# Kernel tuning notes

Measured on AMD Instinct MI355X. Metric: run time of the kernel, lower is better.

The kernel has to match this reference:

```python
import jax, jax.numpy as jnp
import numpy as np

H = 64  # hidden_size
E = 100  # ebd_size
MAX_LEN = 100


def setup_inputs() -> dict:
    key = jax.random.key(0)
    ks = jax.random.split(key, 7)
    B, L = 4096, 100
    return {
        "x": jax.random.normal(ks[0], (B, L, E), jnp.float32),
        "W_in": jax.random.normal(ks[1], (E, 3 * H), jnp.float32) * 0.1,
        "b_in": jax.random.normal(ks[2], (3 * H,), jnp.float32) * 0.1,
        "W_h": jax.random.normal(ks[3], (H, 3 * H), jnp.float32) * 0.1,
        "b_h": jax.random.normal(ks[4], (3 * H,), jnp.float32) * 0.1,
        "W_fc": jax.random.normal(ks[5], (H, 2), jnp.float32) * 0.1,
        "b_fc": jax.random.normal(ks[6], (2,), jnp.float32) * 0.1,
    }


def _standardize(t):
    # torch: (t - t.mean(1, keepdim)) / t.std(1, keepdim)  (std is unbiased, ddof=1)
    m = jnp.mean(t, axis=1, keepdims=True)
    s = jnp.std(t, axis=1, keepdims=True, ddof=1)
    return (t - m) / s


def _gru_step(h, xt, W_in, b_in, W_h, b_h, norm):
    ti = xt @ W_in + b_in            # [B, 3H]
    th = h @ W_h + b_h               # [B, 3H]
    if norm:
        ti = _standardize(ti)
        th = _standardize(th)
    r_i, z_i, n_i = jnp.split(ti, 3, axis=1)
    r_h, z_h, n_h = jnp.split(th, 3, axis=1)
    r_t = jax.nn.sigmoid(r_i + r_h)
    z_t = jax.nn.sigmoid(z_i + z_h)
    n_t = jnp.tanh(n_i + r_t * n_h)
    return (1.0 - z_t) * n_t + z_t * h


def reference(x, W_in, b_in, W_h, b_h, W_fc, b_fc):
    B, L, _ = x.shape
    L_eff = min(L, MAX_LEN + 1)  # loop breaks when l > max_length
    xs = jnp.transpose(x[:, :L_eff, :], (1, 0, 2))  # [L, B, E]
    h0 = jnp.zeros((B, H), x.dtype)

    # loop 1: no norm
    h1, _ = jax.lax.scan(
        lambda h, xt: (_gru_step(h, xt, W_in, b_in, W_h, b_h, norm=False), None),
        h0, xs)
    # loop 2: vector norm; note original code does NOT reset hid_i
    h2, _ = jax.lax.scan(
        lambda h, xt: (_gru_step(h, xt, W_in, b_in, W_h, b_h, norm=True), None),
        h1, xs)
    return h2 @ W_fc + b_fc
```

## Files before the change

kernel.cpp:

```cpp
#include <hip/hip_runtime.h>

#define L_SEQ 100
#define E_DIM 100
#define G_DIM 192
#define B_TOT 4096

typedef __attribute__((ext_vector_type(8))) short bf16x8;
typedef __attribute__((ext_vector_type(4))) float f32x4;
typedef __attribute__((ext_vector_type(4))) float float4v;
typedef __attribute__((ext_vector_type(4))) unsigned uint4v;
typedef __attribute__((ext_vector_type(2))) unsigned uint2v;

static __device__ __forceinline__ unsigned short f2bf(float f) {
    union { float f; unsigned u; } v; v.f = f;
    unsigned r = v.u + 0x7FFFu + ((v.u >> 16) & 1u);
    return (unsigned short)(r >> 16);
}
static __device__ __forceinline__ unsigned cvtpk(float lo, float hi) {
    unsigned r;
    asm("v_cvt_pk_bf16_f32 %0, %1, %2" : "=v"(r) : "v"(lo), "v"(hi));
    return r;
}
static __device__ __forceinline__ bf16x8 as_bf16x8(uint4v u) {
    union { uint4v u; bf16x8 h; } v; v.u = u; return v.h;
}
static __device__ __forceinline__ float sigmoidf_(float x) { return 1.f / (1.f + __expf(-x)); }
static __device__ __forceinline__ float tanhf_(float x)    { return 1.f - 2.f / (__expf(2.f * x) + 1.f); }

#define BAR() do { \
    asm volatile("s_waitcnt lgkmcnt(0)" ::: "memory"); \
    __builtin_amdgcn_s_barrier(); \
    asm volatile("" ::: "memory"); \
} while (0)

struct XBuf { f32x4 v[6]; f32x4 tail; };

static __device__ __forceinline__ void x_pf(
    XBuf& b, const float* __restrict__ xlane, const float* __restrict__ xrow, int s2, bool g0)
{
    int t = (s2 < L_SEQ) ? s2 : (s2 - L_SEQ);
    if (t > L_SEQ - 1) t = L_SEQ - 1;
    const float* p = xlane + t * E_DIM;
    b.v[0] = *(const f32x4*)(p);
    b.v[1] = *(const f32x4*)(p + 4);
    b.v[2] = *(const f32x4*)(p + 32);
    b.v[3] = *(const f32x4*)(p + 36);
    b.v[4] = *(const f32x4*)(p + 64);
    b.v[5] = *(const f32x4*)(p + 68);
    const f32x4 z = {0.f, 0.f, 0.f, 0.f};
    b.tail = g0 ? *(const f32x4*)(xrow + t * E_DIM + 96) : z;
}

template<int PHASE>
static __device__ __forceinline__ void rstep(
    XBuf& xb, const float* __restrict__ xlane, const float* __restrict__ xrow, int s,
    unsigned short (&hs)[2][16][72], float (&sl)[2][16][4][4],
    const bf16x8 (&awin)[3][4], const bf16x8 (&awh)[3][2],
    const float (&binq)[12], const float (&bhq)[12],
    float (&hreg)[4], int w, int g, int c16, bool g0)
{
    bf16x8 bx0 = as_bf16x8((uint4v){cvtpk(xb.v[0][0], xb.v[0][1]), cvtpk(xb.v[0][2], xb.v[0][3]),
                                    cvtpk(xb.v[1][0], xb.v[1][1]), cvtpk(xb.v[1][2], xb.v[1][3])});
    bf16x8 bx1 = as_bf16x8((uint4v){cvtpk(xb.v[2][0], xb.v[2][1]), cvtpk(xb.v[2][2], xb.v[2][3]),
                                    cvtpk(xb.v[3][0], xb.v[3][1]), cvtpk(xb.v[3][2], xb.v[3][3])});
    bf16x8 bx2 = as_bf16x8((uint4v){cvtpk(xb.v[4][0], xb.v[4][1]), cvtpk(xb.v[4][2], xb.v[4][3]),
                                    cvtpk(xb.v[5][0], xb.v[5][1]), cvtpk(xb.v[5][2], xb.v[5][3])});
    bf16x8 bx3 = as_bf16x8((uint4v){cvtpk(xb.tail[0], xb.tail[1]), cvtpk(xb.tail[2], xb.tail[3]),
                                    0u, 0u});
    x_pf(xb, xlane, xrow, s + 2, g0);

    BAR();

    const int p = s & 1;
    bf16x8 h0 = *(const bf16x8*)&hs[p][c16][8 * g];
    bf16x8 h1 = *(const bf16x8*)&hs[p][c16][32 + 8 * g];

    const f32x4 zero = {0.f, 0.f, 0.f, 0.f};
    f32x4 ti0 = __builtin_amdgcn_mfma_f32_16x16x32_bf16(awin[0][0], bx0, zero, 0, 0, 0);
    f32x4 ti1 = __builtin_amdgcn_mfma_f32_16x16x32_bf16(awin[1][0], bx0, zero, 0, 0, 0);
    f32x4 ti2 = __builtin_amdgcn_mfma_f32_16x16x32_bf16(awin[2][0], bx0, zero, 0, 0, 0);
    ti0 = __builtin_amdgcn_mfma_f32_16x16x32_bf16(awin[0][1], bx1, ti0, 0, 0, 0);
    ti1 = __builtin_amdgcn_mfma_f32_16x16x32_bf16(awin[1][1], bx1, ti1, 0, 0, 0);
    ti2 = __builtin_amdgcn_mfma_f32_16x16x32_bf16(awin[2][1], bx1, ti2, 0, 0, 0);
    ti0 = __builtin_amdgcn_mfma_f32_16x16x32_bf16(awin[0][2], bx2, ti0, 0, 0, 0);
    ti1 = __builtin_amdgcn_mfma_f32_16x16x32_bf16(awin[1][2], bx2, ti1, 0, 0, 0);
    ti2 = __builtin_amdgcn_mfma_f32_16x16x32_bf16(awin[2][2], bx2, ti2, 0, 0, 0);
    ti0 = __builtin_amdgcn_mfma_f32_16x16x32_bf16(awin[0][3], bx3, ti0, 0, 0, 0);
    ti1 = __builtin_amdgcn_mfma_f32_16x16x32_bf16(awin[1][3], bx3, ti1, 0, 0, 0);
    ti2 = __builtin_amdgcn_mfma_f32_16x16x32_bf16(awin[2][3], bx3, ti2, 0, 0, 0);
    f32x4 th0 = __builtin_amdgcn_mfma_f32_16x16x32_bf16(awh[0][0], h0, zero, 0, 0, 0);
    f32x4 th1 = __builtin_amdgcn_mfma_f32_16x16x32_bf16(awh[1][0], h0, zero, 0, 0, 0);
    f32x4 th2 = __builtin_amdgcn_mfma_f32_16x16x32_bf16(awh[2][0], h0, zero, 0, 0, 0);
    th0 = __builtin_amdgcn_mfma_f32_16x16x32_bf16(awh[0][1], h1, th0, 0, 0, 0);
    th1 = __builtin_amdgcn_mfma_f32_16x16x32_bf16(awh[1][1], h1, th1, 0, 0, 0);
    th2 = __builtin_amdgcn_mfma_f32_16x16x32_bf16(awh[2][1], h1, th2, 0, 0, 0);

    float a[12], b[12];
    #pragma unroll
    for (int rr = 0; rr < 4; ++rr) {
        a[rr]     = ti0[rr] + binq[rr];
        a[4 + rr] = ti1[rr] + binq[4 + rr];
        a[8 + rr] = ti2[rr] + binq[8 + rr];
        b[rr]     = th0[rr] + bhq[rr];
        b[4 + rr] = th1[rr] + bhq[4 + rr];
        b[8 + rr] = th2[rr] + bhq[8 + rr];
    }

    float mti = 0.f, rti = 1.f, mth = 0.f, rth = 1.f;
    if constexpr (PHASE) {
        float sti = 0.f, ssti = 0.f, sth = 0.f, ssth = 0.f;
        #pragma unroll
        for (int k = 0; k < 12; ++k) {
            sti += a[k]; ssti = fmaf(a[k], a[k], ssti);
            sth += b[k]; ssth = fmaf(b[k], b[k], ssth);
        }
        sti += __shfl_xor(sti, 16); sti += __shfl_xor(sti, 32);
        ssti += __shfl_xor(ssti, 16); ssti += __shfl_xor(ssti, 32);
        sth += __shfl_xor(sth, 16); sth += __shfl_xor(sth, 32);
        ssth += __shfl_xor(ssth, 16); ssth += __shfl_xor(ssth, 32);
        if (g == 0) {
            float4v v = {sti, ssti, sth, ssth};
            *(float4v*)&sl[p][c16][w][0] = v;
        }
        BAR();
        float4v q0 = *(const float4v*)&sl[p][c16][0][0];
        float4v q1 = *(const float4v*)&sl[p][c16][1][0];
        float4v q2 = *(const float4v*)&sl[p][c16][2][0];
        float4v q3 = *(const float4v*)&sl[p][c16][3][0];
        float S_ti  = q0[0] + q1[0] + q2[0] + q3[0];
        float SS_ti = q0[1] + q1[1] + q2[1] + q3[1];
        float S_th  = q0[2] + q1[2] + q2[2] + q3[2];
        float SS_th = q0[3] + q1[3] + q2[3] + q3[3];
        mti = S_ti * (1.f / G_DIM);
        rti = rsqrtf(fmaxf((SS_ti - (float)G_DIM * mti * mti) * (1.f / (G_DIM - 1)), 1e-24f));
        mth = S_th * (1.f / G_DIM);
        rth = rsqrtf(fmaxf((SS_th - (float)G_DIM * mth * mth) * (1.f / (G_DIM - 1)), 1e-24f));
    }

    float hn[4];
    #pragma unroll
    for (int rr = 0; rr < 4; ++rr) {
        float tir, tiz, tin, thr, thz, thn;
        if constexpr (PHASE) {
            tir = (a[rr]     - mti) * rti;
            tiz = (a[4 + rr] - mti) * rti;
            tin = (a[8 + rr] - mti) * rti;
            thr = (b[rr]     - mth) * rth;
            thz = (b[4 + rr] - mth) * rth;
            thn = (b[8 + rr] - mth) * rth;
        } else {
            tir = a[rr]; tiz = a[4 + rr]; tin = a[8 + rr];
            thr = b[rr]; thz = b[4 + rr]; thn = b[8 + rr];
        }
        float rt = sigmoidf_(tir + thr);
        float zt = sigmoidf_(tiz + thz);
        float nv = tanhf_(tin + rt * thn);
        hn[rr] = (1.f - zt) * nv + zt * hreg[rr];
        hreg[rr] = hn[rr];
    }
    uint2v hv = { cvtpk(hn[0], hn[1]), cvtpk(hn[2], hn[3]) };
    *(uint2v*)&hs[p ^ 1][c16][16 * w + 4 * g] = hv;
}

__global__ __launch_bounds__(256, 1) void gru_fused(
    const float* __restrict__ x,
    const float* __restrict__ Win, const float* __restrict__ bin,
    const float* __restrict__ Wh,  const float* __restrict__ bh,
    const float* __restrict__ Wfc, const float* __restrict__ bfc,
    float* __restrict__ out)
{
    __shared__ unsigned short hs[2][16][72];
    __shared__ float sl[2][16][4][4];

    const int tid = threadIdx.x;
    const int w   = tid >> 6, l = tid & 63;
    const int c16 = l & 15,  g = l >> 4;
    const bool g0 = (g == 0);
    const int row0 = blockIdx.x * 16;

    bf16x8 awin[3][4];
    #pragma unroll
    for (int i = 0; i < 3; ++i)
      #pragma unroll
      for (int kt = 0; kt < 4; ++kt)
        #pragma unroll
        for (int j = 0; j < 8; ++j) {
            int k = 32 * kt + 8 * g + j;
            float v = (k < E_DIM) ? Win[k * G_DIM + 16 * (w + 4 * i) + c16] : 0.f;
            awin[i][kt][j] = (short)f2bf(v);
        }
    bf16x8 awh[3][2];
    #pragma unroll
    for (int i = 0; i < 3; ++i)
      #pragma unroll
      for (int kt = 0; kt < 2; ++kt)
        #pragma unroll
        for (int j = 0; j < 8; ++j)
            awh[i][kt][j] = (short)f2bf(Wh[(32 * kt + 8 * g + j) * G_DIM + 16 * (w + 4 * i) + c16]);

    float binq[12], bhq[12];
    #pragma unroll
    for (int i = 0; i < 3; ++i)
      #pragma unroll
      for (int rr = 0; rr < 4; ++rr) {
          binq[4 * i + rr] = bin[16 * (w + 4 * i) + 4 * g + rr];
          bhq[4 * i + rr]  = bh[16 * (w + 4 * i) + 4 * g + rr];
      }

    {
        bf16x8 z = {0, 0, 0, 0, 0, 0, 0, 0};
        *(bf16x8*)&hs[0][c16][8 * g]      = z;
        *(bf16x8*)&hs[0][c16][32 + 8 * g] = z;
    }

    const float* xrow  = x + (size_t)(row0 + c16) * (L_SEQ * E_DIM);
    const float* xlane = xrow + 8 * g;

    float hreg[4] = {0.f, 0.f, 0.f, 0.f};
    XBuf xA, xB;
    x_pf(xA, xlane, xrow, 0, g0);
    x_pf(xB, xlane, xrow, 1, g0);

    #pragma unroll 1
    for (int s = 0; s < L_SEQ; s += 2) {
        rstep<0>(xA, xlane, xrow, s,     hs, sl, awin, awh, binq, bhq, hreg, w, g, c16, g0);
        rstep<0>(xB, xlane, xrow, s + 1, hs, sl, awin, awh, binq, bhq, hreg, w, g, c16, g0);
    }
    #pragma unroll 1
    for (int s = L_SEQ; s < 2 * L_SEQ; s += 2) {
        rstep<1>(xA, xlane, xrow, s,     hs, sl, awin, awh, binq, bhq, hreg, w, g, c16, g0);
        rstep<1>(xB, xlane, xrow, s + 1, hs, sl, awin, awh, binq, bhq, hreg, w, g, c16, g0);
    }

    float p0 = 0.f, p1 = 0.f;
    #pragma unroll
    for (int rr = 0; rr < 4; ++rr) {
        int c = 16 * w + 4 * g + rr;
        p0 = fmaf(hreg[rr], Wfc[2 * c],     p0);
        p1 = fmaf(hreg[rr], Wfc[2 * c + 1], p1);
    }
    p0 += __shfl_xor(p0, 16); p0 += __shfl_xor(p0, 32);
    p1 += __shfl_xor(p1, 16); p1 += __shfl_xor(p1, 32);
    if (g == 0) {
        sl[0][c16][w][0] = p0;
        sl[0][c16][w][1] = p1;
    }
    BAR();
    if (tid < 16) {
        out[(row0 + tid) * 2 + 0] = sl[0][tid][0][0] + sl[0][tid][1][0] + sl[0][tid][2][0] + sl[0][tid][3][0] + bfc[0];
        out[(row0 + tid) * 2 + 1] = sl[0][tid][0][1] + sl[0][tid][1][1] + sl[0][tid][2][1] + sl[0][tid][3][1] + bfc[1];
    }
}

extern "C" void kernel_launch(void* const* d_in, const int* in_sizes, int n_in,
                              void* d_out, int out_size, void* d_ws, size_t ws_size,
                              hipStream_t stream) {
    const float* x   = (const float*)d_in[0];
    const float* Win = (const float*)d_in[1];
    const float* bin = (const float*)d_in[2];
    const float* Wh  = (const float*)d_in[3];
    const float* bh  = (const float*)d_in[4];
    const float* Wfc = (const float*)d_in[5];
    const float* bfc = (const float*)d_in[6];
    float* out = (float*)d_out;
    gru_fused<<<dim3(B_TOT / 16), dim3(256), 0, stream>>>(
        x, Win, bin, Wh, bh, Wfc, bfc, out);
}
```

Baseline: 239.0 us.

## Split GRU into warp-specialized input-projection producer and recurrent consumer waves

Blocks now have 512 threads. Four producer waves compute the input projection x@W_in, including its bias and the sum and sum-of-squares statistics, one step ahead of time and write the results to double-buffered shared memory. Four consumer waves, running at raised priority, do only the h@W_h MFMAs, the normalization and the gate math on the serial recurrence path. The gate math is also rewritten with rcp/rsq intrinsics and fused normalization constants. The aim is to take the x-load and input-GEMM latency off the critical recurrence chain, at the cost of more shared memory, an extra barrier per step and doubled thread count.

Result: faster. 201.0 us (median of 2 runs) (-15.9%).

```diff
diff --git a/kernel.cpp b/kernel.cpp
--- a/kernel.cpp
+++ b/kernel.cpp
@@ -8,8 +8,11 @@
 typedef __attribute__((ext_vector_type(8))) short bf16x8;
 typedef __attribute__((ext_vector_type(4))) float f32x4;
 typedef __attribute__((ext_vector_type(4))) float float4v;
+typedef __attribute__((ext_vector_type(2))) float float2v;
 typedef __attribute__((ext_vector_type(4))) unsigned uint4v;
 typedef __attribute__((ext_vector_type(2))) unsigned uint2v;
+
+#define MFMA16 __builtin_amdgcn_mfma_f32_16x16x32_bf16
 
 static __device__ __forceinline__ unsigned short f2bf(float f) {
     union { float f; unsigned u; } v; v.f = f;
@@ -24,8 +27,7 @@
 static __device__ __forceinline__ bf16x8 as_bf16x8(uint4v u) {
     union { uint4v u; bf16x8 h; } v; v.u = u; return v.h;
 }
-static __device__ __forceinline__ float sigmoidf_(float x) { return 1.f / (1.f + __expf(-x)); }
-static __device__ __forceinline__ float tanhf_(float x)    { return 1.f - 2.f / (__expf(2.f * x) + 1.f); }
+static __device__ __forceinline__ float rcpf_(float x) { return __builtin_amdgcn_rcpf(x); }
 
 #define BAR() do { \
     asm volatile("s_waitcnt lgkmcnt(0)" ::: "memory"); \
@@ -35,11 +37,17 @@
 
 struct XBuf { f32x4 v[6]; f32x4 tail; };
 
+static __device__ __forceinline__ int tmod(int c) {
+    int t = c;
+    if (t >= L_SEQ) t -= L_SEQ;
+    if (t >= L_SEQ) t -= L_SEQ;
+    return t;
+}
+
 static __device__ __forceinline__ void x_pf(
-    XBuf& b, const float* __restrict__ xlane, const float* __restrict__ xrow, int s2, bool g0)
+    XBuf& b, const float* __restrict__ xlane, const float* __restrict__ xrow, int c, bool g0)
 {
-    int t = (s2 < L_SEQ) ? s2 : (s2 - L_SEQ);
-    if (t > L_SEQ - 1) t = L_SEQ - 1;
+    const int t = tmod(c);
     const float* p = xlane + t * E_DIM;
     b.v[0] = *(const f32x4*)(p);
     b.v[1] = *(const f32x4*)(p + 4);
@@ -51,13 +59,10 @@
     b.tail = g0 ? *(const f32x4*)(xrow + t * E_DIM + 96) : z;
 }
 
-template<int PHASE>
-static __device__ __forceinline__ void rstep(
-    XBuf& xb, const float* __restrict__ xlane, const float* __restrict__ xrow, int s,
-    unsigned short (&hs)[2][16][72], float (&sl)[2][16][4][4],
-    const bf16x8 (&awin)[3][4], const bf16x8 (&awh)[3][2],
-    const float (&binq)[12], const float (&bhq)[12],
-    float (&hreg)[4], int w, int g, int c16, bool g0)
+static __device__ __forceinline__ void produce(
+    XBuf& xb, const float* __restrict__ xlane, const float* __restrict__ xrow,
+    int c, bool g0, float* __restrict__ tird, float* __restrict__ sltiw,
+    const bf16x8 (&awin)[3][4], const float (&binq)[12])
 {
     bf16x8 bx0 = as_bf16x8((uint4v){cvtpk(xb.v[0][0], xb.v[0][1]), cvtpk(xb.v[0][2], xb.v[0][3]),
                                     cvtpk(xb.v[1][0], xb.v[1][1]), cvtpk(xb.v[1][2], xb.v[1][3])});
@@ -67,188 +72,253 @@
                                     cvtpk(xb.v[5][0], xb.v[5][1]), cvtpk(xb.v[5][2], xb.v[5][3])});
     bf16x8 bx3 = as_bf16x8((uint4v){cvtpk(xb.tail[0], xb.tail[1]), cvtpk(xb.tail[2], xb.tail[3]),
                                     0u, 0u});
-    x_pf(xb, xlane, xrow, s + 2, g0);
-
-    BAR();
-
-    const int p = s & 1;
-    bf16x8 h0 = *(const bf16x8*)&hs[p][c16][8 * g];
-    bf16x8 h1 = *(const bf16x8*)&hs[p][c16][32 + 8 * g];
+    x_pf(xb, xlane, xrow, c + 2, g0);
 
     const f32x4 zero = {0.f, 0.f, 0.f, 0.f};
-    f32x4 ti0 = __builtin_amdgcn_mfma_f32_16x16x32_bf16(awin[0][0], bx0, zero, 0, 0, 0);
-    f32x4 ti1 = __builtin_amdgcn_mfma_f32_16x16x32_bf16(awin[1][0], bx0, zero, 0, 0, 0);
-    f32x4 ti2 = __builtin_amdgcn_mfma_f32_16x16x32_bf16(awin[2][0], bx0, zero, 0, 0, 0);
-    ti0 = __builtin_amdgcn_mfma_f32_16x16x32_bf16(awin[0][1], bx1, ti0, 0, 0, 0);
-    ti1 = __builtin_amdgcn_mfma_f32_16x16x32_bf16(awin[1][1], bx1, ti1, 0, 0, 0);
-    ti2 = __builtin_amdgcn_mfma_f32_16x16x32_bf16(awin[2][1], bx1, ti2, 0, 0, 0);
-    ti0 = __builtin_amdgcn_mfma_f32_16x16x32_bf16(awin[0][2], bx2, ti0, 0, 0, 0);
-    ti1 = __builtin_amdgcn_mfma_f32_16x16x32_bf16(awin[1][2], bx2, ti1, 0, 0, 0);
-    ti2 = __builtin_amdgcn_mfma_f32_16x16x32_bf16(awin[2][2], bx2, ti2, 0, 0, 0);
-    ti0 = __builtin_amdgcn_mfma_f32_16x16x32_bf16(awin[0][3], bx3, ti0, 0, 0, 0);
-    ti1 = __builtin_amdgcn_mfma_f32_16x16x32_bf16(awin[1][3], bx3, ti1, 0, 0, 0);
-    ti2 = __builtin_amdgcn_mfma_f32_16x16x32_bf16(awin[2][3], bx3, ti2, 0, 0, 0);
-    f32x4 th0 = __builtin_amdgcn_mfma_f32_16x16x32_bf16(awh[0][0], h0, zero, 0, 0, 0);
-    f32x4 th1 = __builtin_amdgcn_mfma_f32_16x16x32_bf16(awh[1][0], h0, zero, 0, 0, 0);
-    f32x4 th2 = __builtin_amdgcn_mfma_f32_16x16x32_bf16(awh[2][0], h0, zero, 0, 0, 0);
-    th0 = __builtin_amdgcn_mfma_f32_16x16x32_bf16(awh[0][1], h1, th0, 0, 0, 0);
-    th1 = __builtin_amdgcn_mfma_f32_16x16x32_bf16(awh[1][1], h1, th1, 0, 0, 0);
-    th2 = __builtin_amdgcn_mfma_f32_16x16x32_bf16(awh[2][1], h1, th2, 0, 0, 0);
-
-    float a[12], b[12];
+    f32x4 t0 = MFMA16(awin[0][0], bx0, zero, 0, 0, 0);
+    f32x4 t1 = MFMA16(awin[1][0], bx0, zero, 0, 0, 0);
+    f32x4 t2 = MFMA16(awin[2][0], bx0, zero, 0, 0, 0);
+    t0 = MFMA16(awin[0][1], bx1, t0, 0, 0, 0);
+    t1 = MFMA16(awin[1][1], bx1, t1, 0, 0, 0);
+    t2 = MFMA16(awin[2][1], bx1, t2, 0, 0, 0);
+    t0 = MFMA16(awin[0][2], bx2, t0, 0, 0, 0);
+    t1 = MFMA16(awin[1][2], bx2, t1, 0, 0, 0);
+    t2 = MFMA16(awin[2][2], bx2, t2, 0, 0, 0);
+    t0 = MFMA16(awin[0][3], bx3, t0, 0, 0, 0);
+    t1 = MFMA16(awin[1][3], bx3, t1, 0, 0, 0);
+    t2 = MFMA16(awin[2][3], bx3, t2, 0, 0, 0);
+
+    const int par = c & 1;
+    float4v A0 = {t0[0] + binq[0], t0[1] + binq[1], t0[2] + binq[2],  t0[3] + binq[3]};
+    float4v A1 = {t1[0] + binq[4], t1[1] + binq[5], t1[2] + binq[6],  t1[3] + binq[7]};
+    float4v A2 = {t2[0] + binq[8], t2[1] + binq[9], t2[2] + binq[10], t2[3] + binq[11]};
+    float* dst = tird + par * 3328;
+    *(float4v*)(dst)     = A0;
+    *(float4v*)(dst + 4) = A1;
+    *(float4v*)(dst + 8) = A2;
+
+    float s = ((A0[0] + A0[1]) + (A0[2] + A0[3])) + ((A1[0] + A1[1]) + (A1[2] + A1[3]))
+            + ((A2[0] + A2[1]) + (A2[2] + A2[3]));
+    float ss = 0.f;
     #pragma unroll
-    for (int rr = 0; rr < 4; ++rr) {
-        a[rr]     = ti0[rr] + binq[rr];
-        a[4 + rr] = ti1[rr] + binq[4 + rr];
-        a[8 + rr] = ti2[rr] + binq[8 + rr];
-        b[rr]     = th0[rr] + bhq[rr];
-        b[4 + rr] = th1[rr] + bhq[4 + rr];
-        b[8 + rr] = th2[rr] + bhq[8 + rr];
-    }
-
-    float mti = 0.f, rti = 1.f, mth = 0.f, rth = 1.f;
-    if constexpr (PHASE) {
-        float sti = 0.f, ssti = 0.f, sth = 0.f, ssth = 0.f;
-        #pragma unroll
-        for (int k = 0; k < 12; ++k) {
-            sti += a[k]; ssti = fmaf(a[k], a[k], ssti);
-            sth += b[k]; ssth = fmaf(b[k], b[k], ssth);
-        }
-        sti += __shfl_xor(sti, 16); sti += __shfl_xor(sti, 32);
-        ssti += __shfl_xor(ssti, 16); ssti += __shfl_xor(ssti, 32);
-        sth += __shfl_xor(sth, 16); sth += __shfl_xor(sth, 32);
-        ssth += __shfl_xor(ssth, 16); ssth += __shfl_xor(ssth, 32);
-        if (g == 0) {
-            float4v v = {sti, ssti, sth, ssth};
-            *(float4v*)&sl[p][c16][w][0] = v;
-        }
-        BAR();
-        float4v q0 = *(const float4v*)&sl[p][c16][0][0];
-        float4v q1 = *(const float4v*)&sl[p][c16][1][0];
-        float4v q2 = *(const float4v*)&sl[p][c16][2][0];
-        float4v q3 = *(const float4v*)&sl[p][c16][3][0];
-        float S_ti  = q0[0] + q1[0] + q2[0] + q3[0];
-        float SS_ti = q0[1] + q1[1] + q2[1] + q3[1];
-        float S_th  = q0[2] + q1[2] + q2[2] + q3[2];
-        float SS_th = q0[3] + q1[3] + q2[3] + q3[3];
-        mti = S_ti * (1.f / G_DIM);
-        rti = rsqrtf(fmaxf((SS_ti - (float)G_DIM * mti * mti) * (1.f / (G_DIM - 1)), 1e-24f));
-        mth = S_th * (1.f / G_DIM);
-        rth = rsqrtf(fmaxf((SS_th - (float)G_DIM * mth * mth) * (1.f / (G_DIM - 1)), 1e-24f));
-    }
-
-    float hn[4];
+    for (int k2 = 0; k2 < 4; ++k2) ss = fmaf(A0[k2], A0[k2], ss);
     #pragma unroll
-    for (int rr = 0; rr < 4; ++rr) {
-        float tir, tiz, tin, thr, thz, thn;
-        if constexpr (PHASE) {
-            tir = (a[rr]     - mti) * rti;
-            tiz = (a[4 + rr] - mti) * rti;
-            tin = (a[8 + rr] - mti) * rti;
-            thr = (b[rr]     - mth) * rth;
-            thz = (b[4 + rr] - mth) * rth;
-            thn = (b[8 + rr] - mth) * rth;
-        } else {
-            tir = a[rr]; tiz = a[4 + rr]; tin = a[8 + rr];
-            thr = b[rr]; thz = b[4 + rr]; thn = b[8 + rr];
-        }
-        float rt = sigmoidf_(tir + thr);
-        float zt = sigmoidf_(tiz + thz);
-        float nv = tanhf_(tin + rt * thn);
-        hn[rr] = (1.f - zt) * nv + zt * hreg[rr];
-        hreg[rr] = hn[rr];
-    }
-    uint2v hv = { cvtpk(hn[0], hn[1]), cvtpk(hn[2], hn[3]) };
-    *(uint2v*)&hs[p ^ 1][c16][16 * w + 4 * g] = hv;
-}
-
-__global__ __launch_bounds__(256, 1) void gru_fused(
+    for (int k2 = 0; k2 < 4; ++k2) ss = fmaf(A1[k2], A1[k2], ss);
+    #pragma unroll
+    for (int k2 = 0; k2 < 4; ++k2) ss = fmaf(A2[k2], A2[k2], ss);
+    s  += __shfl_xor(s, 16);  s  += __shfl_xor(s, 32);
+    ss += __shfl_xor(ss, 16); ss += __shfl_xor(ss, 32);
+    if (g0) *(float2v*)(sltiw + par * 192) = (float2v){s, ss};
+}
+
+__global__ __launch_bounds__(512, 1) void gru_ws(
     const float* __restrict__ x,
     const float* __restrict__ Win, const float* __restrict__ bin,
     const float* __restrict__ Wh,  const float* __restrict__ bh,
     const float* __restrict__ Wfc, const float* __restrict__ bfc,
     float* __restrict__ out)
 {
-    __shared__ unsigned short hs[2][16][72];
-    __shared__ float sl[2][16][4][4];
+    __shared__ __align__(16) unsigned short hs[2][16][72];
+    __shared__ __align__(16) float tir[2][4][16][52];
+    __shared__ __align__(16) float slti[2][16][12];
+    __shared__ __align__(16) float slth[2][16][12];
 
     const int tid = threadIdx.x;
-    const int w   = tid >> 6, l = tid & 63;
-    const int c16 = l & 15,  g = l >> 4;
+    const int wv  = tid >> 6;
+    const int w   = wv & 3;
+    const bool tirole = (wv >= 4);
+    const int l = tid & 63, c16 = l & 15, g = l >> 4;
     const bool g0 = (g == 0);
     const int row0 = blockIdx.x * 16;
 
-    bf16x8 awin[3][4];
-    #pragma unroll
-    for (int i = 0; i < 3; ++i)
-      #pragma unroll
-      for (int kt = 0; kt < 4; ++kt)
-        #pragma unroll
-        for (int j = 0; j < 8; ++j) {
-            int k = 32 * kt + 8 * g + j;
-            float v = (k < E_DIM) ? Win[k * G_DIM + 16 * (w + 4 * i) + c16] : 0.f;
-            awin[i][kt][j] = (short)f2bf(v);
-        }
-    bf16x8 awh[3][2];
-    #pragma unroll
-    for (int i = 0; i < 3; ++i)
-      #pragma unroll
-      for (int kt = 0; kt < 2; ++kt)
-        #pragma unroll
-        for (int j = 0; j < 8; ++j)
-            awh[i][kt][j] = (short)f2bf(Wh[(32 * kt + 8 * g + j) * G_DIM + 16 * (w + 4 * i) + c16]);
-
-    float binq[12], bhq[12];
-    #pragma unroll
-    for (int i = 0; i < 3; ++i)
-      #pragma unroll
-      for (int rr = 0; rr < 4; ++rr) {
-          binq[4 * i + rr] = bin[16 * (w + 4 * i) + 4 * g + rr];
-          bhq[4 * i + rr]  = bh[16 * (w + 4 * i) + 4 * g + rr];
-      }
-
-    {
+    bf16x8 awin[3][4]; float binq[12];
+    bf16x8 awh[3][2];  float bhq[12];
+    const float* xrow = nullptr; const float* xlane = nullptr;
+
+    if (tirole) {
+        #pragma unroll
+        for (int i = 0; i < 3; ++i)
+          #pragma unroll
+          for (int kt = 0; kt < 4; ++kt)
+            #pragma unroll
+            for (int j = 0; j < 8; ++j) {
+                int k = 32 * kt + 8 * g + j;
+                float v = (k < E_DIM) ? Win[k * G_DIM + 16 * (w + 4 * i) + c16] : 0.f;
+                awin[i][kt][j] = (short)f2bf(v);
+            }
+        #pragma unroll
+        for (int i = 0; i < 3; ++i)
+          #pragma unroll
+          for (int rr = 0; rr < 4; ++rr)
+              binq[4 * i + rr] = bin[16 * (w + 4 * i) + 4 * g + rr];
+        xrow  = x + (size_t)(row0 + c16) * (L_SEQ * E_DIM);
+        xlane = xrow + 8 * g;
+    } else {
+        #pragma unroll
+        for (int i = 0; i < 3; ++i)
+          #pragma unroll
+          for (int kt = 0; kt < 2; ++kt)
+            #pragma unroll
+            for (int j = 0; j < 8; ++j)
+                awh[i][kt][j] = (short)f2bf(Wh[(32 * kt + 8 * g + j) * G_DIM + 16 * (w + 4 * i) + c16]);
+        #pragma unroll
+        for (int i = 0; i < 3; ++i)
+          #pragma unroll
+          for (int rr = 0; rr < 4; ++rr)
+              bhq[4 * i + rr] = bh[16 * (w + 4 * i) + 4 * g + rr];
         bf16x8 z = {0, 0, 0, 0, 0, 0, 0, 0};
         *(bf16x8*)&hs[0][c16][8 * g]      = z;
         *(bf16x8*)&hs[0][c16][32 + 8 * g] = z;
     }
 
-    const float* xrow  = x + (size_t)(row0 + c16) * (L_SEQ * E_DIM);
-    const float* xlane = xrow + 8 * g;
+    float* tird        = &tir[0][w][c16][g * 12];
+    float* sltiw       = &slti[0][c16][2 * w];
+    float* slthw       = &slth[0][c16][2 * w];
+    const float* sltir = &slti[0][c16][0];
+    const float* slthr = &slth[0][c16][0];
 
     float hreg[4] = {0.f, 0.f, 0.f, 0.f};
+
     XBuf xA, xB;
-    x_pf(xA, xlane, xrow, 0, g0);
-    x_pf(xB, xlane, xrow, 1, g0);
+    if (tirole) {
+        x_pf(xA, xlane, xrow, 0, g0);
+        x_pf(xB, xlane, xrow, 1, g0);
+        produce(xA, xlane, xrow, 0, g0, tird, sltiw, awin, binq);
+    }
+    BAR();
+    if (!tirole) __builtin_amdgcn_s_setprio(1);
+
+    auto HGEMM = [&](int par, float4v& a0, float4v& a1, float4v& a2, float (&b)[12]) {
+        const float* src = tird + par * 3328;
+        a0 = *(const float4v*)(src);
+        a1 = *(const float4v*)(src + 4);
+        a2 = *(const float4v*)(src + 8);
+        bf16x8 h0 = *(const bf16x8*)&hs[par][c16][8 * g];
+        bf16x8 h1 = *(const bf16x8*)&hs[par][c16][32 + 8 * g];
+        const f32x4 zero = {0.f, 0.f, 0.f, 0.f};
+        f32x4 t0 = MFMA16(awh[0][0], h0, zero, 0, 0, 0);
+        f32x4 t1 = MFMA16(awh[1][0], h0, zero, 0, 0, 0);
+        f32x4 t2 = MFMA16(awh[2][0], h0, zero, 0, 0, 0);
+        t0 = MFMA16(awh[0][1], h1, t0, 0, 0, 0);
+        t1 = MFMA16(awh[1][1], h1, t1, 0, 0, 0);
+        t2 = MFMA16(awh[2][1], h1, t2, 0, 0, 0);
+        #pragma unroll
+        for (int rr = 0; rr < 4; ++rr) {
+            b[rr]     = t0[rr] + bhq[rr];
+            b[4 + rr] = t1[rr] + bhq[4 + rr];
+            b[8 + rr] = t2[rr] + bhq[8 + rr];
+        }
+    };
+    auto HWRITE = [&](int par, float (&hn)[4]) {
+        *(uint2v*)&hs[par ^ 1][c16][16 * w + 4 * g] = (uint2v){cvtpk(hn[0], hn[1]), cvtpk(hn[2], hn[3])};
+    };
 
     #pragma unroll 1
     for (int s = 0; s < L_SEQ; s += 2) {
-        rstep<0>(xA, xlane, xrow, s,     hs, sl, awin, awh, binq, bhq, hreg, w, g, c16, g0);
-        rstep<0>(xB, xlane, xrow, s + 1, hs, sl, awin, awh, binq, bhq, hreg, w, g, c16, g0);
-    }
+        #pragma unroll
+        for (int sub = 0; sub < 2; ++sub) {
+            const int st = s + sub;
+            XBuf& X = sub ? xA : xB;
+            if (tirole) {
+                produce(X, xlane, xrow, st + 1, g0, tird, sltiw, awin, binq);
+            } else {
+                const int par = st & 1;
+                float4v a0, a1, a2; float b[12];
+                HGEMM(par, a0, a1, a2, b);
+                float hn[4];
+                #pragma unroll
+                for (int rr = 0; rr < 4; ++rr) {
+                    float er = rcpf_(1.f + __expf(-(a0[rr] + b[rr])));
+                    float zt = rcpf_(1.f + __expf(-(a1[rr] + b[4 + rr])));
+                    float u  = fmaf(er, b[8 + rr], a2[rr]);
+                    float tn = fmaf(2.f, rcpf_(1.f + __expf(-2.f * u)), -1.f);
+                    hn[rr] = fmaf(zt, hreg[rr] - tn, tn);
+                    hreg[rr] = hn[rr];
+                }
+                HWRITE(par, hn);
+            }
+            BAR();
+        }
+    }
+
     #pragma unroll 1
     for (int s = L_SEQ; s < 2 * L_SEQ; s += 2) {
-        rstep<1>(xA, xlane, xrow, s,     hs, sl, awin, awh, binq, bhq, hreg, w, g, c16, g0);
-        rstep<1>(xB, xlane, xrow, s + 1, hs, sl, awin, awh, binq, bhq, hreg, w, g, c16, g0);
-    }
-
-    float p0 = 0.f, p1 = 0.f;
-    #pragma unroll
-    for (int rr = 0; rr < 4; ++rr) {
-        int c = 16 * w + 4 * g + rr;
-        p0 = fmaf(hreg[rr], Wfc[2 * c],     p0);
-        p1 = fmaf(hreg[rr], Wfc[2 * c + 1], p1);
-    }
-    p0 += __shfl_xor(p0, 16); p0 += __shfl_xor(p0, 32);
-    p1 += __shfl_xor(p1, 16); p1 += __shfl_xor(p1, 32);
-    if (g == 0) {
-        sl[0][c16][w][0] = p0;
-        sl[0][c16][w][1] = p1;
+        #pragma unroll
+        for (int sub = 0; sub < 2; ++sub) {
+            const int st = s + sub;
+            XBuf& X = sub ? xA : xB;
+            const int par = st & 1;
+            float4v a0, a1, a2; float b[12];
+            if (tirole) {
+                produce(X, xlane, xrow, st + 1, g0, tird, sltiw, awin, binq);
+            } else {
+                HGEMM(par, a0, a1, a2, b);
+                float sb = 0.f, ssb = 0.f;
+                #pragma unroll
+                for (int k2 = 0; k2 < 12; ++k2) { sb += b[k2]; ssb = fmaf(b[k2], b[k2], ssb); }
+                sb  += __shfl_xor(sb, 16);  sb  += __shfl_xor(sb, 32);
+                ssb += __shfl_xor(ssb, 16); ssb += __shfl_xor(ssb, 32);
+                if (g0) *(float2v*)(slthw + par * 192) = (float2v){sb, ssb};
+            }
+            BAR();
+            if (!tirole) {
+                const float* sp = slthr + par * 192;
+                float4v q0 = *(const float4v*)(sp);
+                float4v q1 = *(const float4v*)(sp + 4);
+                const float* ip = sltir + par * 192;
+                float4v r0 = *(const float4v*)(ip);
+                float4v r1 = *(const float4v*)(ip + 4);
+                float Sth  = (q0[0] + q0[2]) + (q1[0] + q1[2]);
+                float SSth = (q0[1] + q0[3]) + (q1[1] + q1[3]);
+                float Sti  = (r0[0] + r0[2]) + (r1[0] + r1[2]);
+                float SSti = (r0[1] + r0[3]) + (r1[1] + r1[3]);
+                float mth = Sth * (1.f / G_DIM);
+                float rth = __builtin_amdgcn_rsqf(
+                    fmaxf((SSth - (float)G_DIM * mth * mth) * (1.f / (G_DIM - 1)), 1e-24f));
+                float mti = Sti * (1.f / G_DIM);
+                float rti = __builtin_amdgcn_rsqf(
+                    fmaxf((SSti - (float)G_DIM * mti * mti) * (1.f / (G_DIM - 1)), 1e-24f));
+                float mrti = mti * rti, mrth = mth * rth;
+                float Cn = mrti + mrth;
+                float hn[4];
+                #pragma unroll
+                for (int rr = 0; rr < 4; ++rr) {
+                    float mr = fmaf(a0[rr], -rti, fmaf(b[rr],     -rth, Cn));
+                    float er = rcpf_(1.f + __expf(mr));
+                    float mz = fmaf(a1[rr], -rti, fmaf(b[4 + rr], -rth, Cn));
+                    float zt = rcpf_(1.f + __expf(mz));
+                    float ni = fmaf(a2[rr],     rti, -mrti);
+                    float nh = fmaf(b[8 + rr],  rth, -mrth);
+                    float u  = fmaf(er, nh, ni);
+                    float tn = fmaf(2.f, rcpf_(1.f + __expf(-2.f * u)), -1.f);
+                    hn[rr] = fmaf(zt, hreg[rr] - tn, tn);
+                    hreg[rr] = hn[rr];
+                }
+                HWRITE(par, hn);
+            }
+            BAR();
+        }
+    }
+
+    if (!tirole) {
+        float po0 = 0.f, po1 = 0.f;
+        #pragma unroll
+        for (int rr = 0; rr < 4; ++rr) {
+            int c = 16 * w + 4 * g + rr;
+            po0 = fmaf(hreg[rr], Wfc[2 * c],     po0);
+            po1 = fmaf(hreg[rr], Wfc[2 * c + 1], po1);
+        }
+        po0 += __shfl_xor(po0, 16); po0 += __shfl_xor(po0, 32);
+        po1 += __shfl_xor(po1, 16); po1 += __shfl_xor(po1, 32);
+        if (g0) *(float2v*)(slthw) = (float2v){po0, po1};
     }
     BAR();
     if (tid < 16) {
-        out[(row0 + tid) * 2 + 0] = sl[0][tid][0][0] + sl[0][tid][1][0] + sl[0][tid][2][0] + sl[0][tid][3][0] + bfc[0];
-        out[(row0 + tid) * 2 + 1] = sl[0][tid][0][1] + sl[0][tid][1][1] + sl[0][tid][2][1] + sl[0][tid][3][1] + bfc[1];
+        const float* sp = &slth[0][tid][0];
+        float4v q0 = *(const float4v*)(sp);
+        float4v q1 = *(const float4v*)(sp + 4);
+        out[(row0 + tid) * 2 + 0] = (q0[0] + q0[2]) + (q1[0] + q1[2]) + bfc[0];
+        out[(row0 + tid) * 2 + 1] = (q0[1] + q0[3]) + (q1[1] + q1[3]) + bfc[1];
     }
 }
 
@@ -263,6 +333,6 @@
     const float* Wfc = (const float*)d_in[5];
     const float* bfc = (const float*)d_in[6];
     float* out = (float*)d_out;
-    gru_fused<<<dim3(B_TOT / 16), dim3(256), 0, stream>>>(
+    gru_ws<<<dim3(B_TOT / 16), dim3(512), 0, stream>>>(
         x, Win, bin, Wh, bh, Wfc, bfc, out);
 }
```
